# Kernel optimization log

Measured on AMD Instinct MI355X. Metric: run time of the kernel, lower is better.

The kernel has to match this reference:

```python
import jax, jax.numpy as jnp
import numpy as np

T_LEN = 1024
N_IN = 512
BATCH = 32
SURR_ALPHA = 4.0  # slope of the sigmoid surrogate gradient


@jax.custom_vjp
def heaviside_sg(x):
    # spike = Heaviside(x); backward uses sigmoid surrogate derivative
    return (x >= 0).astype(x.dtype)

def _hs_fwd(x):
    return heaviside_sg(x), x

def _hs_bwd(x, g):
    s = jax.nn.sigmoid(SURR_ALPHA * x)
    return (g * SURR_ALPHA * s * (1.0 - s),)

heaviside_sg.defvjp(_hs_fwd, _hs_bwd)


def setup_inputs() -> dict:
    key = jax.random.key(0)
    k1, k2, k3 = jax.random.split(key, 3)
    current = jax.random.normal(k1, (T_LEN, BATCH, N_IN), dtype=jnp.float32)
    beta = jax.random.uniform(k2, (N_IN,), dtype=jnp.float32)  # per-channel decay in (0,1)
    v_init = jax.random.normal(k3, (BATCH, N_IN), dtype=jnp.float32)
    v_th = jnp.ones((T_LEN, BATCH, N_IN), dtype=jnp.float32)
    return {"current": current, "beta": beta, "v_init": v_init, "v_th": v_th}


def reference(current, beta, v_init, v_th):
    # Torch version: grouped causal conv1d with kernel beta^{T-1-k}, i.e.
    # membrane[t] = sum_{j<=t} beta^{t-j} * current[j], with current[0] += beta*v_init.
    # Equivalent O(T) linear recurrence: m_t = beta*m_{t-1} + c_t, m_{-1}=v_init.
    def step(m, c):
        m = beta * m + c  # beta (N,) broadcasts over (B,N)
        return m, m

    m_last, membrane = jax.lax.scan(step, v_init, current)  # membrane: (T,B,N)

    # surrogate-gradient spike function
    spikes = heaviside_sg(membrane - v_th)  # (T,B,N)

    # triangular phi kernel: z[t] = sum_{j<=t} (t-j+1)*spikes[j] == double cumsum
    z = jnp.cumsum(jnp.cumsum(spikes, axis=0), axis=0)  # (T,B,N)

    # Block.g: keep entries equal to 1, zero everything else; gradient is identity
    # (the subtracted term is detached in the torch code).
    gz = z - jax.lax.stop_gradient(jnp.where(z == 1.0, 0.0, z))

    return gz, z, m_last  # m_last == membrane[:, :, -1] in torch layout (B,N)
```

## Files before the change

### kernel.cpp

```cpp
#include <hip/hip_runtime.h>


#define T_LEN 1024
#define N_IN  512
#define BN    16384
#define U     16

struct Buf { float c[U]; float v[U]; };

__device__ __forceinline__ void prefetch(Buf& b, const float* __restrict__ cp,
                                         const float* __restrict__ vp, int t0) {
    const float* __restrict__ c = cp + t0 * BN;
    const float* __restrict__ v = vp + t0 * BN;
#pragma unroll
    for (int u = 0; u < U; ++u) {
        b.c[u] = c[u * BN];
        b.v[u] = v[u * BN];
    }
}

__device__ __forceinline__ void process(const Buf& b, float beta, float& m, int& c1,
                                        int& z, float* __restrict__ gp,
                                        float* __restrict__ zp, int t0) {
#pragma unroll
    for (int u = 0; u < U; ++u) {
        m = fmaf(beta, m, b.c[u]);
        c1 += (m >= b.v[u]) ? 1 : 0;
        z  += c1;
        gp[(t0 + u) * BN] = (z == 1) ? 1.0f : 0.0f;
        zp[(t0 + u) * BN] = (float)z;
    }
}

__global__ __launch_bounds__(64, 1) void snn_scan(
        const float* __restrict__ cur, const float* __restrict__ beta,
        const float* __restrict__ vini, const float* __restrict__ vth,
        float* __restrict__ gz, float* __restrict__ zo, float* __restrict__ ml)
{
    const int i = blockIdx.x * 64 + threadIdx.x;
    const float bta = beta[i & (N_IN - 1)];
    float m = vini[i];
    int c1 = 0, z = 0;

    const float* cp = cur + i;
    const float* vp = vth + i;
    float* gp = gz + i;
    float* zp = zo + i;

    Buf b0, b1, b2, b3;
    prefetch(b0, cp, vp, 0);
    prefetch(b1, cp, vp, U);
    prefetch(b2, cp, vp, 2 * U);
    prefetch(b3, cp, vp, 3 * U);

    for (int t0 = 0; t0 < T_LEN; t0 += 4 * U) {
        process(b0, bta, m, c1, z, gp, zp, t0);
        if (t0 + 4 * U < T_LEN) prefetch(b0, cp, vp, t0 + 4 * U);
        process(b1, bta, m, c1, z, gp, zp, t0 + U);
        if (t0 + 5 * U < T_LEN) prefetch(b1, cp, vp, t0 + 5 * U);
        process(b2, bta, m, c1, z, gp, zp, t0 + 2 * U);
        if (t0 + 6 * U < T_LEN) prefetch(b2, cp, vp, t0 + 6 * U);
        process(b3, bta, m, c1, z, gp, zp, t0 + 3 * U);
        if (t0 + 7 * U < T_LEN) prefetch(b3, cp, vp, t0 + 7 * U);
    }
    ml[i] = m;
}

extern "C" void kernel_launch(void* const* d_in, const int* in_sizes, int n_in,
                              void* d_out, int out_size, void* d_ws, size_t ws_size,
                              hipStream_t stream) {
    const float* cur  = (const float*)d_in[0];
    const float* beta = (const float*)d_in[1];
    const float* vini = (const float*)d_in[2];
    const float* vth  = (const float*)d_in[3];
    float* gz = (float*)d_out;
    float* zo = gz + (size_t)T_LEN * BN;
    float* ml = zo + (size_t)T_LEN * BN;
    snn_scan<<<BN / 64, 64, 0, stream>>>(cur, beta, vini, vth, gz, zo, ml);
}
```

Before: 249.2 us.

## Split scan into spike-bitmask phase and parallel multi-wave output writers

Wave 0 of each block runs the membrane recurrence and packs spike results into 32-bit masks in shared memory, no longer storing the two large outputs itself. After a barrier, eight waves each replay the prefix counts up to their time segment from the bitmasks and write their 128-step slice of gz and z. This spreads the store traffic, which dominates the output volume, over more waves to raise memory parallelism. In exchange the serial recurrence now runs alone before any stores begin, and later waves repeat the prefix popcount work.

```diff
diff --git a/kernel.cpp b/kernel.cpp
--- a/kernel.cpp
+++ b/kernel.cpp
@@ -10,60 +10,89 @@
 
 __device__ __forceinline__ void prefetch(Buf& b, const float* __restrict__ cp,
                                          const float* __restrict__ vp, int t0) {
-    const float* __restrict__ c = cp + t0 * BN;
-    const float* __restrict__ v = vp + t0 * BN;
+    const float* __restrict__ c = cp + (size_t)t0 * BN;
+    const float* __restrict__ v = vp + (size_t)t0 * BN;
 #pragma unroll
     for (int u = 0; u < U; ++u) {
-        b.c[u] = c[u * BN];
-        b.v[u] = v[u * BN];
+        b.c[u] = c[(size_t)u * BN];
+        b.v[u] = v[(size_t)u * BN];
     }
 }
 
-__device__ __forceinline__ void process(const Buf& b, float beta, float& m, int& c1,
-                                        int& z, float* __restrict__ gp,
-                                        float* __restrict__ zp, int t0) {
+__device__ __forceinline__ unsigned process16(const Buf& b, float beta, float& m) {
+    unsigned mask = 0u;
 #pragma unroll
     for (int u = 0; u < U; ++u) {
         m = fmaf(beta, m, b.c[u]);
-        c1 += (m >= b.v[u]) ? 1 : 0;
-        z  += c1;
-        gp[(t0 + u) * BN] = (z == 1) ? 1.0f : 0.0f;
-        zp[(t0 + u) * BN] = (float)z;
+        mask |= (m >= b.v[u]) ? (1u << u) : 0u;
     }
+    return mask;
 }
 
-__global__ __launch_bounds__(64, 1) void snn_scan(
+__global__ __launch_bounds__(512, 2) void snn_scan(
         const float* __restrict__ cur, const float* __restrict__ beta,
         const float* __restrict__ vini, const float* __restrict__ vth,
         float* __restrict__ gz, float* __restrict__ zo, float* __restrict__ ml)
 {
-    const int i = blockIdx.x * 64 + threadIdx.x;
-    const float bta = beta[i & (N_IN - 1)];
-    float m = vini[i];
-    int c1 = 0, z = 0;
+    __shared__ unsigned bits[T_LEN / 32][64];
 
-    const float* cp = cur + i;
-    const float* vp = vth + i;
-    float* gp = gz + i;
-    float* zp = zo + i;
+    const int lane = threadIdx.x & 63;
+    const int wave = threadIdx.x >> 6;
+    const int i = blockIdx.x * 64 + lane;
 
-    Buf b0, b1, b2, b3;
-    prefetch(b0, cp, vp, 0);
-    prefetch(b1, cp, vp, U);
-    prefetch(b2, cp, vp, 2 * U);
-    prefetch(b3, cp, vp, 3 * U);
+    if (wave == 0) {
+        const float bta = beta[i & (N_IN - 1)];
+        float m = vini[i];
+        const float* cp = cur + i;
+        const float* vp = vth + i;
 
-    for (int t0 = 0; t0 < T_LEN; t0 += 4 * U) {
-        process(b0, bta, m, c1, z, gp, zp, t0);
-        if (t0 + 4 * U < T_LEN) prefetch(b0, cp, vp, t0 + 4 * U);
-        process(b1, bta, m, c1, z, gp, zp, t0 + U);
-        if (t0 + 5 * U < T_LEN) prefetch(b1, cp, vp, t0 + 5 * U);
-        process(b2, bta, m, c1, z, gp, zp, t0 + 2 * U);
-        if (t0 + 6 * U < T_LEN) prefetch(b2, cp, vp, t0 + 6 * U);
-        process(b3, bta, m, c1, z, gp, zp, t0 + 3 * U);
-        if (t0 + 7 * U < T_LEN) prefetch(b3, cp, vp, t0 + 7 * U);
+        Buf b0, b1, b2, b3;
+        prefetch(b0, cp, vp, 0);
+        prefetch(b1, cp, vp, U);
+        prefetch(b2, cp, vp, 2 * U);
+        prefetch(b3, cp, vp, 3 * U);
+
+        for (int t0 = 0; t0 < T_LEN; t0 += 4 * U) {
+            unsigned m0 = process16(b0, bta, m);
+            if (t0 + 4 * U < T_LEN) prefetch(b0, cp, vp, t0 + 4 * U);
+            unsigned m1 = process16(b1, bta, m);
+            if (t0 + 5 * U < T_LEN) prefetch(b1, cp, vp, t0 + 5 * U);
+            bits[t0 >> 5][lane] = m0 | (m1 << 16);
+            unsigned m2 = process16(b2, bta, m);
+            if (t0 + 6 * U < T_LEN) prefetch(b2, cp, vp, t0 + 6 * U);
+            unsigned m3 = process16(b3, bta, m);
+            if (t0 + 7 * U < T_LEN) prefetch(b3, cp, vp, t0 + 7 * U);
+            bits[(t0 >> 5) + 1][lane] = m2 | (m3 << 16);
+        }
+        ml[i] = m;
     }
-    ml[i] = m;
+    __syncthreads();
+
+    int C = 0;
+    int Z = 0;
+    const int d0 = wave * 4;
+    for (int d = 0; d < d0; ++d) {
+        unsigned u = bits[d][lane];
+#pragma unroll
+        for (int b = 0; b < 32; ++b) {
+            C += (u >> b) & 1u;
+            Z += C;
+        }
+    }
+
+    float* __restrict__ gp = gz + (size_t)(d0 * 32) * BN + i;
+    float* __restrict__ zp = zo + (size_t)(d0 * 32) * BN + i;
+    for (int d = 0; d < 4; ++d) {
+        unsigned u = bits[d0 + d][lane];
+#pragma unroll
+        for (int b = 0; b < 32; ++b) {
+            C += (u >> b) & 1u;
+            Z += C;
+            const size_t off = (size_t)(d * 32 + b) * BN;
+            gp[off] = (Z == 1) ? 1.0f : 0.0f;
+            zp[off] = (float)Z;
+        }
+    }
 }
 
 extern "C" void kernel_launch(void* const* d_in, const int* in_sizes, int n_in,
@@ -76,5 +105,5 @@
     float* gz = (float*)d_out;
     float* zo = gz + (size_t)T_LEN * BN;
     float* ml = zo + (size_t)T_LEN * BN;
-    snn_scan<<<BN / 64, 64, 0, stream>>>(cur, beta, vini, vth, gz, zo, ml);
+    snn_scan<<<BN / 64, 512, 0, stream>>>(cur, beta, vini, vth, gz, zo, ml);
 }
```

Result: no change. 247.1 us (-0.8%).

## Warp-specialize scan: LDS async loads, single scan wave, eight writer waves

Applied to the files above, without the earlier changes.

The one-wave-per-block scan becomes a warp-specialized block of 11 waves. Two producer waves stream current and threshold segments into double-buffered LDS with global_load_lds. One wave runs the serial recurrence and packs spikes into bitmasks with prefix counts. Eight writer waves rebuild the double cumsum per timestep and emit float4 stores for both outputs. The aim is to overlap memory traffic with the serial scan and widen stores, at the cost of a block barrier per 32-step segment and redundant bit-replay work in the writers.

```diff
diff --git a/kernel.cpp b/kernel.cpp
--- a/kernel.cpp
+++ b/kernel.cpp
@@ -4,66 +4,117 @@
 #define T_LEN 1024
 #define N_IN  512
 #define BN    16384
-#define U     16
+#define SEG_T 32
+#define NSEG  (T_LEN / SEG_T)
 
-struct Buf { float c[U]; float v[U]; };
+__device__ __forceinline__ void gload_lds16(const float* g, float* l) {
+    __builtin_amdgcn_global_load_lds(
+        (const __attribute__((address_space(1))) void*)g,
+        (__attribute__((address_space(3))) void*)l, 16, 0, 0);
+}
 
-__device__ __forceinline__ void prefetch(Buf& b, const float* __restrict__ cp,
-                                         const float* __restrict__ vp, int t0) {
-    const float* __restrict__ c = cp + t0 * BN;
-    const float* __restrict__ v = vp + t0 * BN;
+__device__ __forceinline__ void issue_seg(const float* __restrict__ src,
+                                          float* dst, int s, size_t goff) {
 #pragma unroll
-    for (int u = 0; u < U; ++u) {
-        b.c[u] = c[u * BN];
-        b.v[u] = v[u * BN];
+    for (int j = 0; j < SEG_T / 4; ++j) {
+        gload_lds16(src + (size_t)(SEG_T * s + 4 * j) * BN + goff, dst + j * 256);
     }
 }
 
-__device__ __forceinline__ void process(const Buf& b, float beta, float& m, int& c1,
-                                        int& z, float* __restrict__ gp,
-                                        float* __restrict__ zp, int t0) {
-#pragma unroll
-    for (int u = 0; u < U; ++u) {
-        m = fmaf(beta, m, b.c[u]);
-        c1 += (m >= b.v[u]) ? 1 : 0;
-        z  += c1;
-        gp[(t0 + u) * BN] = (z == 1) ? 1.0f : 0.0f;
-        zp[(t0 + u) * BN] = (float)z;
-    }
-}
-
-__global__ __launch_bounds__(64, 1) void snn_scan(
+__global__ __launch_bounds__(704, 1) void snn_fused(
         const float* __restrict__ cur, const float* __restrict__ beta,
         const float* __restrict__ vini, const float* __restrict__ vth,
         float* __restrict__ gz, float* __restrict__ zo, float* __restrict__ ml)
 {
-    const int i = blockIdx.x * 64 + threadIdx.x;
-    const float bta = beta[i & (N_IN - 1)];
-    float m = vini[i];
-    int c1 = 0, z = 0;
+    __shared__ float    ldsC[2][SEG_T * 64];
+    __shared__ float    ldsV[2][SEG_T * 64];
+    __shared__ unsigned bitsb[2][64];
+    __shared__ unsigned pcb[2][64];
 
-    const float* cp = cur + i;
-    const float* vp = vth + i;
-    float* gp = gz + i;
-    float* zp = zo + i;
+    const int lane   = threadIdx.x & 63;
+    const int wave   = threadIdx.x >> 6;
+    const int chbase = blockIdx.x * 64;
+    const size_t goff = (size_t)chbase + (size_t)(lane >> 4) * BN
+                      + (size_t)(4 * (lane & 15));
 
-    Buf b0, b1, b2, b3;
-    prefetch(b0, cp, vp, 0);
-    prefetch(b1, cp, vp, U);
-    prefetch(b2, cp, vp, 2 * U);
-    prefetch(b3, cp, vp, 3 * U);
+    float bta = 0.0f, m = 0.0f;
+    int C = 0, Z = 0;
+    if (wave == 0) {
+        bta = beta[(chbase + lane) & (N_IN - 1)];
+        m   = vini[chbase + lane];
+    }
 
-    for (int t0 = 0; t0 < T_LEN; t0 += 4 * U) {
-        process(b0, bta, m, c1, z, gp, zp, t0);
-        if (t0 + 4 * U < T_LEN) prefetch(b0, cp, vp, t0 + 4 * U);
-        process(b1, bta, m, c1, z, gp, zp, t0 + U);
-        if (t0 + 5 * U < T_LEN) prefetch(b1, cp, vp, t0 + 5 * U);
-        process(b2, bta, m, c1, z, gp, zp, t0 + 2 * U);
-        if (t0 + 6 * U < T_LEN) prefetch(b2, cp, vp, t0 + 6 * U);
-        process(b3, bta, m, c1, z, gp, zp, t0 + 3 * U);
-        if (t0 + 7 * U < T_LEN) prefetch(b3, cp, vp, t0 + 7 * U);
+    const int ww      = wave - 3;
+    const int row_sub = lane >> 4;
+    const int chgrp   = lane & 15;
+    const int myrow   = 4 * ww + row_sub;
+
+    if (wave == 1) issue_seg(cur, &ldsC[0][0], 0, goff);
+    if (wave == 2) issue_seg(vth, &ldsV[0][0], 0, goff);
+    __syncthreads();
+
+    for (int s = 0; s <= NSEG; ++s) {
+        if (wave == 1 && s + 1 < NSEG) issue_seg(cur, &ldsC[(s + 1) & 1][0], s + 1, goff);
+        if (wave == 2 && s + 1 < NSEG) issue_seg(vth, &ldsV[(s + 1) & 1][0], s + 1, goff);
+
+        if (wave == 0 && s < NSEG) {
+            const int cb = s & 1;
+            pcb[cb][lane] = (unsigned)C | ((unsigned)Z << 11);
+            const float* lc = &ldsC[cb][lane];
+            const float* lv = &ldsV[cb][lane];
+            float cc[SEG_T], vv[SEG_T];
+#pragma unroll
+            for (int t = 0; t < SEG_T; ++t) {
+                cc[t] = lc[t * 64];
+                vv[t] = lv[t * 64];
+            }
+            unsigned mask = 0u;
+#pragma unroll
+            for (int t = 0; t < SEG_T; ++t) {
+                m = fmaf(bta, m, cc[t]);
+                const int sp = (m >= vv[t]) ? 1 : 0;
+                mask |= (unsigned)sp << t;
+                C += sp;
+                Z += C;
+            }
+            bitsb[cb][lane] = mask;
+            if (s == NSEG - 1) ml[chbase + lane] = m;
+        }
+
+        if (wave >= 3 && s >= 1) {
+            const int ds = s - 1;
+            const int pb = ds & 1;
+            const uint4 ub = *reinterpret_cast<const uint4*>(&bitsb[pb][4 * chgrp]);
+            const uint4 pp = *reinterpret_cast<const uint4*>(&pcb[pb][4 * chgrp]);
+            int C0 = (int)(pp.x & 0x7FFu), Z0 = (int)(pp.x >> 11);
+            int C1 = (int)(pp.y & 0x7FFu), Z1 = (int)(pp.y >> 11);
+            int C2 = (int)(pp.z & 0x7FFu), Z2 = (int)(pp.z >> 11);
+            int C3 = (int)(pp.w & 0x7FFu), Z3 = (int)(pp.w >> 11);
+            int zq0 = 0, zq1 = 0, zq2 = 0, zq3 = 0;
+            const int tmax = 4 * ww + 4;
+            for (int t = 0; t < tmax; ++t) {
+                C0 += (int)((ub.x >> t) & 1u); Z0 += C0;
+                C1 += (int)((ub.y >> t) & 1u); Z1 += C1;
+                C2 += (int)((ub.z >> t) & 1u); Z2 += C2;
+                C3 += (int)((ub.w >> t) & 1u); Z3 += C3;
+                zq0 = (t == myrow) ? Z0 : zq0;
+                zq1 = (t == myrow) ? Z1 : zq1;
+                zq2 = (t == myrow) ? Z2 : zq2;
+                zq3 = (t == myrow) ? Z3 : zq3;
+            }
+            const size_t off = (size_t)(ds * 32 + myrow) * BN + chbase + 4 * chgrp;
+            const float4 gf = make_float4(zq0 == 1 ? 1.0f : 0.0f,
+                                          zq1 == 1 ? 1.0f : 0.0f,
+                                          zq2 == 1 ? 1.0f : 0.0f,
+                                          zq3 == 1 ? 1.0f : 0.0f);
+            const float4 zf = make_float4((float)zq0, (float)zq1,
+                                          (float)zq2, (float)zq3);
+            *reinterpret_cast<float4*>(gz + off) = gf;
+            *reinterpret_cast<float4*>(zo + off) = zf;
+        }
+
+        if (s < NSEG) __syncthreads();
     }
-    ml[i] = m;
 }
 
 extern "C" void kernel_launch(void* const* d_in, const int* in_sizes, int n_in,
@@ -76,5 +127,6 @@
     float* gz = (float*)d_out;
     float* zo = gz + (size_t)T_LEN * BN;
     float* ml = zo + (size_t)T_LEN * BN;
-    snn_scan<<<BN / 64, 64, 0, stream>>>(cur, beta, vini, vth, gz, zo, ml);
+
+    snn_fused<<<BN / 64, 704, 0, stream>>>(cur, beta, vini, vth, gz, zo, ml);
 }
```

Result: no change. 250.4 us (+0.5%).
